# Kernel tuning notes

Hardware: AMD Instinct MI355X
Metric: run time of the kernel (lower is better)

## Reference

```python
import jax, jax.numpy as jnp
import numpy as np

N_NODES = 100000
N_EDGES = 1600000
IN_CH, HID, N_CLS = 768, 256, 8


def setup_inputs() -> dict:
    key = jax.random.key(0)
    k1, k2, k3, k4 = jax.random.split(key, 4)
    x = jax.random.normal(k1, (N_NODES, IN_CH), dtype=jnp.float32)
    edge_index = jax.random.randint(k2, (2, N_EDGES), 0, N_NODES, dtype=jnp.int64)
    # Glorot-ish init scaled for stability
    W1 = jax.random.normal(k3, (IN_CH, HID), dtype=jnp.float32) * (1.0 / np.sqrt(IN_CH))
    b1 = jnp.zeros((HID,), dtype=jnp.float32)
    W2 = jax.random.normal(k4, (HID, N_CLS), dtype=jnp.float32) * (1.0 / np.sqrt(HID))
    b2 = jnp.zeros((N_CLS,), dtype=jnp.float32)
    return {"x": x, "edge_index": edge_index, "W1": W1, "b1": b1, "W2": W2, "b2": b2}


def _gcn_norm(edge_index, num_nodes):
    # Add self-loops (PyG GCNConv default) and compute symmetric normalization.
    loops = jnp.arange(num_nodes, dtype=edge_index.dtype)
    row = jnp.concatenate([edge_index[0], loops])  # source nodes
    col = jnp.concatenate([edge_index[1], loops])  # target nodes
    ones = jnp.ones(col.shape[0], dtype=jnp.float32)
    deg = jax.ops.segment_sum(ones, col, num_segments=num_nodes)
    dinv = jnp.where(deg > 0, jax.lax.rsqrt(deg), 0.0)
    norm = dinv[row] * dinv[col]  # [E + N]
    return row, col, norm


def _gcn_conv(x, row, col, norm, W, b):
    h = x @ W                      # [N, out] dense transform first (out <= in)
    msg = h[row] * norm[:, None]    # gather + scale, [E+N, out]
    agg = jax.ops.segment_sum(msg, col, num_segments=x.shape[0])  # scatter-add
    return agg + b


def reference(x, edge_index, W1, b1, W2, b2):
    row, col, norm = _gcn_norm(edge_index, x.shape[0])
    h = _gcn_conv(x, row, col, norm, W1, b1)
    h = jax.nn.relu(h)
    # dropout is identity at eval (training=False)
    out = _gcn_conv(h, row, col, norm, W2, b2)
    return out
```

## Files before the change

### kernel.cpp

```cpp
#include <hip/hip_runtime.h>


#define NN 100000
#define NE 1600000
#define INC 768
#define HID 256
#define NCLS 8
#define NBLK 391

typedef short bf16x8 __attribute__((ext_vector_type(8)));
typedef float f32x4 __attribute__((ext_vector_type(4)));

__device__ __forceinline__ unsigned short f2bf(float f) {
  unsigned int u = __float_as_uint(f);
  unsigned int r = (u + 0x7FFFu + ((u >> 16) & 1u)) >> 16;
  return (unsigned short)r;
}
__device__ __forceinline__ float bf2f(unsigned short h) {
  return __uint_as_float(((unsigned int)h) << 16);
}

__global__ __launch_bounds__(256) void k_count(const int* __restrict__ ei, int* __restrict__ cnt) {
  int e = blockIdx.x * 256 + threadIdx.x;
  if (e < NE) atomicAdd(&cnt[ei[NE + e]], 1);
}

__global__ __launch_bounds__(256) void k_scan1(const int* __restrict__ cnt, int* __restrict__ bsum,
                                               float* __restrict__ dinv) {
  __shared__ int s[256];
  int i = blockIdx.x * 256 + threadIdx.x;
  int v = (i < NN) ? cnt[i] : 0;
  if (i < NN) dinv[i] = rsqrtf((float)v + 1.0f);
  s[threadIdx.x] = v;
  __syncthreads();
#pragma unroll
  for (int off = 128; off > 0; off >>= 1) {
    if (threadIdx.x < off) s[threadIdx.x] += s[threadIdx.x + off];
    __syncthreads();
  }
  if (threadIdx.x == 0) bsum[blockIdx.x] = s[0];
}
__global__ __launch_bounds__(512) void k_scan2(const int* __restrict__ bsum, int* __restrict__ boff,
                                               int* __restrict__ rowptr) {
  __shared__ int s[512];
  int tid = threadIdx.x;
  int v = (tid < NBLK) ? bsum[tid] : 0;
  s[tid] = v;
  __syncthreads();
#pragma unroll
  for (int off = 1; off < 512; off <<= 1) {
    int t = (tid >= off) ? s[tid - off] : 0;
    __syncthreads();
    s[tid] += t;
    __syncthreads();
  }
  if (tid < NBLK) boff[tid] = s[tid] - v;
  if (tid == NBLK - 1) rowptr[NN] = s[tid];
}
__global__ __launch_bounds__(256) void k_scan3(const int* __restrict__ cnt, const int* __restrict__ boff,
                                               int* __restrict__ rowptr, int* __restrict__ cursor) {
  __shared__ int s[256];
  int i = blockIdx.x * 256 + threadIdx.x;
  int v = (i < NN) ? cnt[i] : 0;
  s[threadIdx.x] = v;
  __syncthreads();
#pragma unroll
  for (int off = 1; off < 256; off <<= 1) {
    int t = (threadIdx.x >= off) ? s[threadIdx.x - off] : 0;
    __syncthreads();
    s[threadIdx.x] += t;
    __syncthreads();
  }
  if (i < NN) {
    int e = boff[blockIdx.x] + s[threadIdx.x] - v;
    rowptr[i] = e;
    cursor[i] = e;
  }
}
__global__ __launch_bounds__(256) void k_fill(const int* __restrict__ ei, const float* __restrict__ dinv,
                                              int* __restrict__ cursor, int2* __restrict__ epk) {
  int e = blockIdx.x * 256 + threadIdx.x;
  if (e >= NE) return;
  int r = ei[e];
  int c = ei[NE + e];
  float w = dinv[r] * dinv[c];
  int pos = atomicAdd(&cursor[c], 1);
  epk[pos] = make_int2(r, __float_as_int(w));
}

__global__ __launch_bounds__(256) void k_w1t(const float* __restrict__ W1, unsigned short* __restrict__ w1t) {
  int t = blockIdx.x * 256 + threadIdx.x;
  if (t >= INC * HID) return;
  int k = t / HID, n = t % HID;
  w1t[n * INC + k] = f2bf(W1[t]);
}

__global__ __launch_bounds__(512) void k_gemm1(const float* __restrict__ x,
                                               const unsigned short* __restrict__ w1t,
                                               unsigned short* __restrict__ h1) {
  __shared__ char smem[49152];
  unsigned short* As = (unsigned short*)smem;
  unsigned short* Bs = (unsigned short*)(smem + 16384);
  const int tid = threadIdx.x;
  const int lane = tid & 63;
  const int wid = tid >> 6;
  const int wm = wid >> 2;
  const int wn = wid & 3;
  const long bm = blockIdx.x;

  const int ar0 = tid >> 3, as7 = tid & 7;
  const int ar1 = (tid + 512) >> 3;
  long arow0 = bm * 128 + ar0; if (arow0 > NN - 1) arow0 = NN - 1;
  long arow1 = bm * 128 + ar1; if (arow1 > NN - 1) arow1 = NN - 1;
  const float* gA0 = x + arow0 * INC + as7 * 8;
  const float* gA1 = x + arow1 * INC + as7 * 8;
  const int aoff0 = (ar0 << 7) | ((as7 ^ (ar0 & 7)) << 4);
  const int aoff1 = (ar1 << 7) | ((as7 ^ (ar1 & 7)) << 4);

  f32x4 acc[4][4];
#pragma unroll
  for (int m = 0; m < 4; m++)
#pragma unroll
    for (int n = 0; n < 4; n++) acc[m][n] = (f32x4){0.f, 0.f, 0.f, 0.f};

  float4 fa00, fa01, fa10, fa11;
  uint4 rb0, rb1, rb2, rb3;

#define LOAD_AB(KT)                                                        \
  do {                                                                     \
    fa00 = *(const float4*)(gA0 + (KT));                                   \
    fa01 = *(const float4*)(gA0 + (KT) + 4);                               \
    fa10 = *(const float4*)(gA1 + (KT));                                   \
    fa11 = *(const float4*)(gA1 + (KT) + 4);                               \
    rb0 = *(const uint4*)(w1t + (long)(tid >> 3) * INC + (KT) + (tid & 7) * 8);            \
    rb1 = *(const uint4*)(w1t + (long)((tid + 512) >> 3) * INC + (KT) + (tid & 7) * 8);    \
    rb2 = *(const uint4*)(w1t + (long)((tid + 1024) >> 3) * INC + (KT) + (tid & 7) * 8);   \
    rb3 = *(const uint4*)(w1t + (long)((tid + 1536) >> 3) * INC + (KT) + (tid & 7) * 8);   \
  } while (0)

  LOAD_AB(0);

  for (int kt = 0; kt < INC; kt += 64) {
    {
      union { unsigned short us[8]; uint4 v; } u;
      u.us[0] = f2bf(fa00.x); u.us[1] = f2bf(fa00.y); u.us[2] = f2bf(fa00.z); u.us[3] = f2bf(fa00.w);
      u.us[4] = f2bf(fa01.x); u.us[5] = f2bf(fa01.y); u.us[6] = f2bf(fa01.z); u.us[7] = f2bf(fa01.w);
      *(uint4*)((char*)As + aoff0) = u.v;
      u.us[0] = f2bf(fa10.x); u.us[1] = f2bf(fa10.y); u.us[2] = f2bf(fa10.z); u.us[3] = f2bf(fa10.w);
      u.us[4] = f2bf(fa11.x); u.us[5] = f2bf(fa11.y); u.us[6] = f2bf(fa11.z); u.us[7] = f2bf(fa11.w);
      *(uint4*)((char*)As + aoff1) = u.v;
    }
    {
      int r0 = tid >> 3, s7 = tid & 7;
      *(uint4*)((char*)Bs + ((r0 << 7) | ((s7 ^ (r0 & 7)) << 4))) = rb0;
      int r1 = (tid + 512) >> 3;
      *(uint4*)((char*)Bs + ((r1 << 7) | ((s7 ^ (r1 & 7)) << 4))) = rb1;
      int r2 = (tid + 1024) >> 3;
      *(uint4*)((char*)Bs + ((r2 << 7) | ((s7 ^ (r2 & 7)) << 4))) = rb2;
      int r3 = (tid + 1536) >> 3;
      *(uint4*)((char*)Bs + ((r3 << 7) | ((s7 ^ (r3 & 7)) << 4))) = rb3;
    }
    __syncthreads();
    if (kt + 64 < INC) LOAD_AB(kt + 64);
#pragma unroll
    for (int half = 0; half < 2; half++) {
      bf16x8 af[4], bff[4];
      int j = (half << 2) + (lane >> 4);
#pragma unroll
      for (int m = 0; m < 4; m++) {
        int row = wm * 64 + m * 16 + (lane & 15);
        int off = (row << 7) | ((j ^ (row & 7)) << 4);
        af[m] = *(const bf16x8*)((const char*)As + off);
      }
#pragma unroll
      for (int n = 0; n < 4; n++) {
        int row = wn * 64 + n * 16 + (lane & 15);
        int off = (row << 7) | ((j ^ (row & 7)) << 4);
        bff[n] = *(const bf16x8*)((const char*)Bs + off);
      }
#pragma unroll
      for (int m = 0; m < 4; m++)
#pragma unroll
        for (int n = 0; n < 4; n++)
          acc[m][n] = __builtin_amdgcn_mfma_f32_16x16x32_bf16(af[m], bff[n], acc[m][n], 0, 0, 0);
    }
    __syncthreads();
  }
#undef LOAD_AB

  unsigned short* Os = (unsigned short*)smem;
#pragma unroll
  for (int chunk = 0; chunk < 2; chunk++) {
    if (wm == chunk) {
#pragma unroll
      for (int m = 0; m < 4; m++)
#pragma unroll
        for (int n = 0; n < 4; n++) {
          int lrow = m * 16 + ((lane >> 4) << 2);
          int lcol = wn * 64 + n * 16 + (lane & 15);
#pragma unroll
          for (int r = 0; r < 4; r++)
            Os[(lrow + r) * 264 + lcol] = f2bf(acc[m][n][r]);
        }
    }
    __syncthreads();
    {
      int r = tid >> 3, s = tid & 7;
      long grow = bm * 128 + chunk * 64 + r;
      if (grow < NN) {
        unsigned short* dst = h1 + grow * HID;
#pragma unroll
        for (int i = 0; i < 4; i++) {
          int seg = s + i * 8;
          *(uint4*)(dst + seg * 8) = *(const uint4*)((const char*)Os + (long)r * 528 + seg * 16);
        }
      }
    }
    __syncthreads();
  }
}

__global__ __launch_bounds__(256) void k_agg1(const unsigned short* __restrict__ h1,
                                              const float* __restrict__ dinv,
                                              const int* __restrict__ rowptr,
                                              const int2* __restrict__ epk,
                                              const float* __restrict__ b1,
                                              const float* __restrict__ W2,
                                              float* __restrict__ h2) {
  int w = (int)((blockIdx.x * 256 + threadIdx.x) >> 6);
  int lane = threadIdx.x & 63;
  if (w >= NN) return;
  float di = dinv[w];
  int c4 = lane << 2;
  const unsigned short* hb = h1 + c4;
  ushort4 hv = *(const ushort4*)(hb + (long)w * HID);
  float self = di * di;
  float a0 = self * bf2f(hv.x), a1 = self * bf2f(hv.y);
  float a2 = self * bf2f(hv.z), a3 = self * bf2f(hv.w);
  int e = rowptr[w], e1 = rowptr[w + 1];
  if ((e & 1) && e < e1) {
    int2 q = epk[e];
    float ws = __int_as_float(q.y);
    ushort4 g = *(const ushort4*)(hb + (long)q.x * HID);
    a0 += ws * bf2f(g.x); a1 += ws * bf2f(g.y);
    a2 += ws * bf2f(g.z); a3 += ws * bf2f(g.w);
    e++;
  }
  for (; e + 8 <= e1; e += 8) {
    uint4 p0 = *(const uint4*)(epk + e);
    uint4 p1 = *(const uint4*)(epk + e + 2);
    uint4 p2 = *(const uint4*)(epk + e + 4);
    uint4 p3 = *(const uint4*)(epk + e + 6);
    ushort4 g0 = *(const ushort4*)(hb + (long)(int)p0.x * HID);
    ushort4 g1 = *(const ushort4*)(hb + (long)(int)p0.z * HID);
    ushort4 g2 = *(const ushort4*)(hb + (long)(int)p1.x * HID);
    ushort4 g3 = *(const ushort4*)(hb + (long)(int)p1.z * HID);
    ushort4 g4 = *(const ushort4*)(hb + (long)(int)p2.x * HID);
    ushort4 g5 = *(const ushort4*)(hb + (long)(int)p2.z * HID);
    ushort4 g6 = *(const ushort4*)(hb + (long)(int)p3.x * HID);
    ushort4 g7 = *(const ushort4*)(hb + (long)(int)p3.z * HID);
    float w0 = __uint_as_float(p0.y), w1 = __uint_as_float(p0.w);
    float w2 = __uint_as_float(p1.y), w3 = __uint_as_float(p1.w);
    float w4 = __uint_as_float(p2.y), w5 = __uint_as_float(p2.w);
    float w6 = __uint_as_float(p3.y), w7 = __uint_as_float(p3.w);
    a0 += w0 * bf2f(g0.x) + w1 * bf2f(g1.x) + w2 * bf2f(g2.x) + w3 * bf2f(g3.x) +
          w4 * bf2f(g4.x) + w5 * bf2f(g5.x) + w6 * bf2f(g6.x) + w7 * bf2f(g7.x);
    a1 += w0 * bf2f(g0.y) + w1 * bf2f(g1.y) + w2 * bf2f(g2.y) + w3 * bf2f(g3.y) +
          w4 * bf2f(g4.y) + w5 * bf2f(g5.y) + w6 * bf2f(g6.y) + w7 * bf2f(g7.y);
    a2 += w0 * bf2f(g0.z) + w1 * bf2f(g1.z) + w2 * bf2f(g2.z) + w3 * bf2f(g3.z) +
          w4 * bf2f(g4.z) + w5 * bf2f(g5.z) + w6 * bf2f(g6.z) + w7 * bf2f(g7.z);
    a3 += w0 * bf2f(g0.w) + w1 * bf2f(g1.w) + w2 * bf2f(g2.w) + w3 * bf2f(g3.w) +
          w4 * bf2f(g4.w) + w5 * bf2f(g5.w) + w6 * bf2f(g6.w) + w7 * bf2f(g7.w);
  }
  for (; e + 2 <= e1; e += 2) {
    uint4 p = *(const uint4*)(epk + e);
    ushort4 g0 = *(const ushort4*)(hb + (long)(int)p.x * HID);
    ushort4 g1 = *(const ushort4*)(hb + (long)(int)p.z * HID);
    float w0 = __uint_as_float(p.y), w1 = __uint_as_float(p.w);
    a0 += w0 * bf2f(g0.x) + w1 * bf2f(g1.x);
    a1 += w0 * bf2f(g0.y) + w1 * bf2f(g1.y);
    a2 += w0 * bf2f(g0.z) + w1 * bf2f(g1.z);
    a3 += w0 * bf2f(g0.w) + w1 * bf2f(g1.w);
  }
  if (e < e1) {
    int2 q = epk[e];
    float ws = __int_as_float(q.y);
    ushort4 g = *(const ushort4*)(hb + (long)q.x * HID);
    a0 += ws * bf2f(g.x); a1 += ws * bf2f(g.y);
    a2 += ws * bf2f(g.z); a3 += ws * bf2f(g.w);
  }
  float4 bv = *(const float4*)(b1 + c4);
  float v0 = a0 + bv.x; v0 = v0 > 0.f ? v0 : 0.f;
  float v1 = a1 + bv.y; v1 = v1 > 0.f ? v1 : 0.f;
  float v2 = a2 + bv.z; v2 = v2 > 0.f ? v2 : 0.f;
  float v3 = a3 + bv.w; v3 = v3 > 0.f ? v3 : 0.f;
  const float4* wp = (const float4*)(W2 + ((long)c4 << 3));
  float4 r0a = wp[0], r0b = wp[1], r1a = wp[2], r1b = wp[3];
  float4 r2a = wp[4], r2b = wp[5], r3a = wp[6], r3b = wp[7];
  float p[8];
  p[0] = v0 * r0a.x + v1 * r1a.x + v2 * r2a.x + v3 * r3a.x;
  p[1] = v0 * r0a.y + v1 * r1a.y + v2 * r2a.y + v3 * r3a.y;
  p[2] = v0 * r0a.z + v1 * r1a.z + v2 * r2a.z + v3 * r3a.z;
  p[3] = v0 * r0a.w + v1 * r1a.w + v2 * r2a.w + v3 * r3a.w;
  p[4] = v0 * r0b.x + v1 * r1b.x + v2 * r2b.x + v3 * r3b.x;
  p[5] = v0 * r0b.y + v1 * r1b.y + v2 * r2b.y + v3 * r3b.y;
  p[6] = v0 * r0b.z + v1 * r1b.z + v2 * r2b.z + v3 * r3b.z;
  p[7] = v0 * r0b.w + v1 * r1b.w + v2 * r2b.w + v3 * r3b.w;
#pragma unroll
  for (int c = 0; c < 8; c++)
#pragma unroll
    for (int off = 1; off < 64; off <<= 1) p[c] += __shfl_xor(p[c], off, 64);
  if (lane < 8) {
    float o = p[0];
    o = (lane == 1) ? p[1] : o;
    o = (lane == 2) ? p[2] : o;
    o = (lane == 3) ? p[3] : o;
    o = (lane == 4) ? p[4] : o;
    o = (lane == 5) ? p[5] : o;
    o = (lane == 6) ? p[6] : o;
    o = (lane == 7) ? p[7] : o;
    h2[(long)w * NCLS + lane] = o;
  }
}

__global__ __launch_bounds__(256) void k_agg2(const float* __restrict__ h2,
                                              const float* __restrict__ dinv,
                                              const int* __restrict__ rowptr,
                                              const int2* __restrict__ epk,
                                              const float* __restrict__ b2,
                                              float* __restrict__ out) {
  long t = (long)blockIdx.x * 256 + threadIdx.x;
  long i = t >> 3;
  int c = (int)(t & 7);
  if (i >= NN) return;
  float di = dinv[i];
  float s = di * di * h2[i * NCLS + c];
  int e = rowptr[i], e1 = rowptr[i + 1];
  for (; e + 8 <= e1; e += 8) {
    int2 q0 = epk[e],     q1 = epk[e + 1], q2 = epk[e + 2], q3 = epk[e + 3];
    int2 q4 = epk[e + 4], q5 = epk[e + 5], q6 = epk[e + 6], q7 = epk[e + 7];
    float g0 = h2[(long)q0.x * NCLS + c], g1 = h2[(long)q1.x * NCLS + c];
    float g2 = h2[(long)q2.x * NCLS + c], g3 = h2[(long)q3.x * NCLS + c];
    float g4 = h2[(long)q4.x * NCLS + c], g5 = h2[(long)q5.x * NCLS + c];
    float g6 = h2[(long)q6.x * NCLS + c], g7 = h2[(long)q7.x * NCLS + c];
    s += __int_as_float(q0.y) * g0 + __int_as_float(q1.y) * g1 +
         __int_as_float(q2.y) * g2 + __int_as_float(q3.y) * g3 +
         __int_as_float(q4.y) * g4 + __int_as_float(q5.y) * g5 +
         __int_as_float(q6.y) * g6 + __int_as_float(q7.y) * g7;
  }
  for (; e < e1; e++) {
    int2 q = epk[e];
    s += __int_as_float(q.y) * h2[(long)q.x * NCLS + c];
  }
  out[i * NCLS + c] = s + b2[c];
}

extern "C" void kernel_launch(void* const* d_in, const int* in_sizes, int n_in,
                              void* d_out, int out_size, void* d_ws, size_t ws_size,
                              hipStream_t stream) {
  (void)in_sizes; (void)n_in; (void)out_size; (void)ws_size;
  const float* x  = (const float*)d_in[0];
  const int*   ei = (const int*)d_in[1];
  const float* W1 = (const float*)d_in[2];
  const float* b1 = (const float*)d_in[3];
  const float* W2 = (const float*)d_in[4];
  const float* b2 = (const float*)d_in[5];
  float* out = (float*)d_out;
  char* ws = (char*)d_ws;

  unsigned short* h1   = (unsigned short*)(ws + 0L);
  float* h2            = (float*)(ws + 51200000L);
  float* dinv          = (float*)(ws + 54400000L);
  int*   cnt           = (int*)(ws + 54800000L);
  int*   rowptr        = (int*)(ws + 55200000L);
  int*   cursor        = (int*)(ws + 55600128L);
  int2*  epk           = (int2*)(ws + 56000128L);
  unsigned short* w1t  = (unsigned short*)(ws + 68800128L);
  int*   bsum          = (int*)(ws + 69195008L);
  int*   boff          = (int*)(ws + 69196608L);

  hipMemsetAsync(cnt, 0, NN * sizeof(int), stream);
  k_count<<<(NE + 255) / 256, 256, 0, stream>>>(ei, cnt);
  k_scan1<<<NBLK, 256, 0, stream>>>(cnt, bsum, dinv);
  k_scan2<<<1, 512, 0, stream>>>(bsum, boff, rowptr);
  k_scan3<<<NBLK, 256, 0, stream>>>(cnt, boff, rowptr, cursor);
  k_fill<<<(NE + 255) / 256, 256, 0, stream>>>(ei, dinv, cursor, epk);
  k_w1t<<<(INC * HID + 255) / 256, 256, 0, stream>>>(W1, w1t);
  k_gemm1<<<782, 512, 0, stream>>>(x, w1t, h1);
  k_agg1<<<(NN * 64 + 255) / 256, 256, 0, stream>>>(h1, dinv, rowptr, epk, b1, W2, h2);
  k_agg2<<<(NN * NCLS + 255) / 256, 256, 0, stream>>>(h2, dinv, rowptr, epk, b2, out);
}
```

Before: 458.0 us.

## Double-buffer GEMM1 LDS tiles with half-size K steps

Splits the 64-wide K tile of the first GEMM into two 32-wide tiles held in separate LDS buffers. Each one is written while MFMAs run on the other, so staging overlaps compute and the barrier wait between store and compute shrinks. Register prefetch now holds half as much data per thread, which lowers register pressure. In exchange the LDS swizzle is narrower, and the kernel issues more barriers and smaller global loads per iteration.

```diff
diff --git a/kernel.cpp b/kernel.cpp
--- a/kernel.cpp
+++ b/kernel.cpp
@@ -99,8 +99,10 @@
                                                const unsigned short* __restrict__ w1t,
                                                unsigned short* __restrict__ h1) {
   __shared__ char smem[49152];
-  unsigned short* As = (unsigned short*)smem;
-  unsigned short* Bs = (unsigned short*)(smem + 16384);
+  unsigned short* A0 = (unsigned short*)smem;
+  unsigned short* A1 = (unsigned short*)(smem + 8192);
+  unsigned short* B0 = (unsigned short*)(smem + 16384);
+  unsigned short* B1 = (unsigned short*)(smem + 32768);
   const int tid = threadIdx.x;
   const int lane = tid & 63;
   const int wid = tid >> 6;
@@ -108,14 +110,16 @@
   const int wn = wid & 3;
   const long bm = blockIdx.x;
 
-  const int ar0 = tid >> 3, as7 = tid & 7;
-  const int ar1 = (tid + 512) >> 3;
-  long arow0 = bm * 128 + ar0; if (arow0 > NN - 1) arow0 = NN - 1;
-  long arow1 = bm * 128 + ar1; if (arow1 > NN - 1) arow1 = NN - 1;
-  const float* gA0 = x + arow0 * INC + as7 * 8;
-  const float* gA1 = x + arow1 * INC + as7 * 8;
-  const int aoff0 = (ar0 << 7) | ((as7 ^ (ar0 & 7)) << 4);
-  const int aoff1 = (ar1 << 7) | ((as7 ^ (ar1 & 7)) << 4);
+  const int ar = tid >> 2, ak = tid & 3;
+  long arow = bm * 128 + ar; if (arow > NN - 1) arow = NN - 1;
+  const float* gA = x + arow * INC + ak * 8;
+  const int aoff = (ar << 6) | ((ak ^ (ar & 3)) << 4);
+  const int br0 = tid >> 2;
+  const int br1 = (tid + 512) >> 2;
+  const unsigned short* gB0 = w1t + (long)br0 * INC + ak * 8;
+  const unsigned short* gB1 = w1t + (long)br1 * INC + ak * 8;
+  const int boff0 = (br0 << 6) | ((ak ^ (br0 & 3)) << 4);
+  const int boff1 = (br1 << 6) | ((ak ^ (br1 & 3)) << 4);
 
   f32x4 acc[4][4];
 #pragma unroll
@@ -123,70 +127,70 @@
 #pragma unroll
     for (int n = 0; n < 4; n++) acc[m][n] = (f32x4){0.f, 0.f, 0.f, 0.f};
 
-  float4 fa00, fa01, fa10, fa11;
-  uint4 rb0, rb1, rb2, rb3;
-
-#define LOAD_AB(KT)                                                        \
-  do {                                                                     \
-    fa00 = *(const float4*)(gA0 + (KT));                                   \
-    fa01 = *(const float4*)(gA0 + (KT) + 4);                               \
-    fa10 = *(const float4*)(gA1 + (KT));                                   \
-    fa11 = *(const float4*)(gA1 + (KT) + 4);                               \
-    rb0 = *(const uint4*)(w1t + (long)(tid >> 3) * INC + (KT) + (tid & 7) * 8);            \
-    rb1 = *(const uint4*)(w1t + (long)((tid + 512) >> 3) * INC + (KT) + (tid & 7) * 8);    \
-    rb2 = *(const uint4*)(w1t + (long)((tid + 1024) >> 3) * INC + (KT) + (tid & 7) * 8);   \
-    rb3 = *(const uint4*)(w1t + (long)((tid + 1536) >> 3) * INC + (KT) + (tid & 7) * 8);   \
+  float4 fa0, fa1;
+  uint4 rb0, rb1;
+
+#define LOAD_T(KT)                              \
+  do {                                          \
+    fa0 = *(const float4*)(gA + (KT));          \
+    fa1 = *(const float4*)(gA + (KT) + 4);      \
+    rb0 = *(const uint4*)(gB0 + (KT));          \
+    rb1 = *(const uint4*)(gB1 + (KT));          \
   } while (0)
 
-  LOAD_AB(0);
-
-  for (int kt = 0; kt < INC; kt += 64) {
-    {
-      union { unsigned short us[8]; uint4 v; } u;
-      u.us[0] = f2bf(fa00.x); u.us[1] = f2bf(fa00.y); u.us[2] = f2bf(fa00.z); u.us[3] = f2bf(fa00.w);
-      u.us[4] = f2bf(fa01.x); u.us[5] = f2bf(fa01.y); u.us[6] = f2bf(fa01.z); u.us[7] = f2bf(fa01.w);
-      *(uint4*)((char*)As + aoff0) = u.v;
-      u.us[0] = f2bf(fa10.x); u.us[1] = f2bf(fa10.y); u.us[2] = f2bf(fa10.z); u.us[3] = f2bf(fa10.w);
-      u.us[4] = f2bf(fa11.x); u.us[5] = f2bf(fa11.y); u.us[6] = f2bf(fa11.z); u.us[7] = f2bf(fa11.w);
-      *(uint4*)((char*)As + aoff1) = u.v;
+#define WRITE_T(AB, BB)                                                          \
+  do {                                                                           \
+    union { unsigned short us[8]; uint4 v; } u;                                  \
+    u.us[0] = f2bf(fa0.x); u.us[1] = f2bf(fa0.y); u.us[2] = f2bf(fa0.z);         \
+    u.us[3] = f2bf(fa0.w); u.us[4] = f2bf(fa1.x); u.us[5] = f2bf(fa1.y);         \
+    u.us[6] = f2bf(fa1.z); u.us[7] = f2bf(fa1.w);                                \
+    *(uint4*)((char*)(AB) + aoff) = u.v;                                         \
+    *(uint4*)((char*)(BB) + boff0) = rb0;                                        \
+    *(uint4*)((char*)(BB) + boff1) = rb1;                                        \
+  } while (0)
+
+#define MFMA_T(AB, BB)                                                           \
+  do {                                                                           \
+    bf16x8 af[4], bff[4];                                                        \
+    int j = lane >> 4;                                                           \
+    _Pragma("unroll")                                                            \
+    for (int m = 0; m < 4; m++) {                                                \
+      int row = wm * 64 + m * 16 + (lane & 15);                                  \
+      af[m] = *(const bf16x8*)((const char*)(AB) + ((row << 6) | ((j ^ (row & 3)) << 4))); \
+    }                                                                            \
+    _Pragma("unroll")                                                            \
+    for (int n = 0; n < 4; n++) {                                                \
+      int row = wn * 64 + n * 16 + (lane & 15);                                  \
+      bff[n] = *(const bf16x8*)((const char*)(BB) + ((row << 6) | ((j ^ (row & 3)) << 4))); \
+    }                                                                            \
+    _Pragma("unroll")                                                            \
+    for (int m = 0; m < 4; m++)                                                  \
+      _Pragma("unroll")                                                          \
+      for (int n = 0; n < 4; n++)                                                \
+        acc[m][n] = __builtin_amdgcn_mfma_f32_16x16x32_bf16(af[m], bff[n], acc[m][n], 0, 0, 0); \
+  } while (0)
+
+  LOAD_T(0);
+  WRITE_T(A0, B0);
+  LOAD_T(32);
+  __syncthreads();
+
+  for (int u = 0; u < 12; u++) {
+    int kt = u * 64;
+    WRITE_T(A1, B1);
+    if (kt + 64 < INC) LOAD_T(kt + 64);
+    MFMA_T(A0, B0);
+    __syncthreads();
+    if (kt + 64 < INC) {
+      WRITE_T(A0, B0);
+      if (kt + 96 < INC) LOAD_T(kt + 96);
     }
-    {
-      int r0 = tid >> 3, s7 = tid & 7;
-      *(uint4*)((char*)Bs + ((r0 << 7) | ((s7 ^ (r0 & 7)) << 4))) = rb0;
-      int r1 = (tid + 512) >> 3;
-      *(uint4*)((char*)Bs + ((r1 << 7) | ((s7 ^ (r1 & 7)) << 4))) = rb1;
-      int r2 = (tid + 1024) >> 3;
-      *(uint4*)((char*)Bs + ((r2 << 7) | ((s7 ^ (r2 & 7)) << 4))) = rb2;
-      int r3 = (tid + 1536) >> 3;
-      *(uint4*)((char*)Bs + ((r3 << 7) | ((s7 ^ (r3 & 7)) << 4))) = rb3;
-    }
-    __syncthreads();
-    if (kt + 64 < INC) LOAD_AB(kt + 64);
-#pragma unroll
-    for (int half = 0; half < 2; half++) {
-      bf16x8 af[4], bff[4];
-      int j = (half << 2) + (lane >> 4);
-#pragma unroll
-      for (int m = 0; m < 4; m++) {
-        int row = wm * 64 + m * 16 + (lane & 15);
-        int off = (row << 7) | ((j ^ (row & 7)) << 4);
-        af[m] = *(const bf16x8*)((const char*)As + off);
-      }
-#pragma unroll
-      for (int n = 0; n < 4; n++) {
-        int row = wn * 64 + n * 16 + (lane & 15);
-        int off = (row << 7) | ((j ^ (row & 7)) << 4);
-        bff[n] = *(const bf16x8*)((const char*)Bs + off);
-      }
-#pragma unroll
-      for (int m = 0; m < 4; m++)
-#pragma unroll
-        for (int n = 0; n < 4; n++)
-          acc[m][n] = __builtin_amdgcn_mfma_f32_16x16x32_bf16(af[m], bff[n], acc[m][n], 0, 0, 0);
-    }
-    __syncthreads();
-  }
-#undef LOAD_AB
+    MFMA_T(A1, B1);
+    __syncthreads();
+  }
+#undef LOAD_T
+#undef WRITE_T
+#undef MFMA_T
 
   unsigned short* Os = (unsigned short*)smem;
 #pragma unroll
```

Measured after the change: 482.3 us. 1.05x slower.

## Restructure GEMM1 to stream W1 from global in MFMA-ready layout, no LDS staging

Applied to the files above, without the earlier changes.

The first GEMM no longer stages A and B tiles through shared memory with barriers. Each wave now owns 16 rows and all 256 output columns. It reads x directly into registers and loads W1 fragments from global memory, using a new pre-packed [k/8][n][8] layout that matches the MFMA operand shape. This removes the LDS traffic and the __syncthreads per k-tile. In exchange, every wave re-reads the whole of W1 from L2/cache, uses 64 accumulator registers, and gets less B reuse per block. The bf16 conversion now uses the HIP intrinsic instead of hand-written rounding.

```diff
diff --git a/kernel.cpp b/kernel.cpp
--- a/kernel.cpp
+++ b/kernel.cpp
@@ -1,4 +1,5 @@
 #include <hip/hip_runtime.h>
+#include <hip/hip_bf16.h>
 
 
 #define NN 100000
@@ -12,9 +13,8 @@
 typedef float f32x4 __attribute__((ext_vector_type(4)));
 
 __device__ __forceinline__ unsigned short f2bf(float f) {
-  unsigned int u = __float_as_uint(f);
-  unsigned int r = (u + 0x7FFFu + ((u >> 16) & 1u)) >> 16;
-  return (unsigned short)r;
+  __hip_bfloat16 h = __float2bfloat16(f);
+  return *reinterpret_cast<unsigned short*>(&h);
 }
 __device__ __forceinline__ float bf2f(unsigned short h) {
   return __uint_as_float(((unsigned int)h) << 16);
@@ -88,135 +88,70 @@
   epk[pos] = make_int2(r, __float_as_int(w));
 }
 
-__global__ __launch_bounds__(256) void k_w1t(const float* __restrict__ W1, unsigned short* __restrict__ w1t) {
+__global__ __launch_bounds__(256) void k_w1t(const float* __restrict__ W1, unsigned short* __restrict__ w1t2) {
   int t = blockIdx.x * 256 + threadIdx.x;
   if (t >= INC * HID) return;
   int k = t / HID, n = t % HID;
-  w1t[n * INC + k] = f2bf(W1[t]);
-}
-
-__global__ __launch_bounds__(512) void k_gemm1(const float* __restrict__ x,
-                                               const unsigned short* __restrict__ w1t,
+  w1t2[(k >> 3) * (HID * 8) + n * 8 + (k & 7)] = f2bf(W1[t]);
+}
+
+__global__ __launch_bounds__(256) void k_gemm1(const float* __restrict__ x,
+                                               const unsigned short* __restrict__ w1t2,
                                                unsigned short* __restrict__ h1) {
-  __shared__ char smem[49152];
-  unsigned short* As = (unsigned short*)smem;
-  unsigned short* Bs = (unsigned short*)(smem + 16384);
+  __shared__ unsigned short Os[64 * 264];
   const int tid = threadIdx.x;
   const int lane = tid & 63;
-  const int wid = tid >> 6;
-  const int wm = wid >> 2;
-  const int wn = wid & 3;
-  const long bm = blockIdx.x;
-
-  const int ar0 = tid >> 3, as7 = tid & 7;
-  const int ar1 = (tid + 512) >> 3;
-  long arow0 = bm * 128 + ar0; if (arow0 > NN - 1) arow0 = NN - 1;
-  long arow1 = bm * 128 + ar1; if (arow1 > NN - 1) arow1 = NN - 1;
-  const float* gA0 = x + arow0 * INC + as7 * 8;
-  const float* gA1 = x + arow1 * INC + as7 * 8;
-  const int aoff0 = (ar0 << 7) | ((as7 ^ (ar0 & 7)) << 4);
-  const int aoff1 = (ar1 << 7) | ((as7 ^ (ar1 & 7)) << 4);
-
-  f32x4 acc[4][4];
-#pragma unroll
-  for (int m = 0; m < 4; m++)
-#pragma unroll
-    for (int n = 0; n < 4; n++) acc[m][n] = (f32x4){0.f, 0.f, 0.f, 0.f};
-
-  float4 fa00, fa01, fa10, fa11;
-  uint4 rb0, rb1, rb2, rb3;
-
-#define LOAD_AB(KT)                                                        \
-  do {                                                                     \
-    fa00 = *(const float4*)(gA0 + (KT));                                   \
-    fa01 = *(const float4*)(gA0 + (KT) + 4);                               \
-    fa10 = *(const float4*)(gA1 + (KT));                                   \
-    fa11 = *(const float4*)(gA1 + (KT) + 4);                               \
-    rb0 = *(const uint4*)(w1t + (long)(tid >> 3) * INC + (KT) + (tid & 7) * 8);            \
-    rb1 = *(const uint4*)(w1t + (long)((tid + 512) >> 3) * INC + (KT) + (tid & 7) * 8);    \
-    rb2 = *(const uint4*)(w1t + (long)((tid + 1024) >> 3) * INC + (KT) + (tid & 7) * 8);   \
-    rb3 = *(const uint4*)(w1t + (long)((tid + 1536) >> 3) * INC + (KT) + (tid & 7) * 8);   \
-  } while (0)
-
-  LOAD_AB(0);
-
-  for (int kt = 0; kt < INC; kt += 64) {
-    {
-      union { unsigned short us[8]; uint4 v; } u;
-      u.us[0] = f2bf(fa00.x); u.us[1] = f2bf(fa00.y); u.us[2] = f2bf(fa00.z); u.us[3] = f2bf(fa00.w);
-      u.us[4] = f2bf(fa01.x); u.us[5] = f2bf(fa01.y); u.us[6] = f2bf(fa01.z); u.us[7] = f2bf(fa01.w);
-      *(uint4*)((char*)As + aoff0) = u.v;
-      u.us[0] = f2bf(fa10.x); u.us[1] = f2bf(fa10.y); u.us[2] = f2bf(fa10.z); u.us[3] = f2bf(fa10.w);
-      u.us[4] = f2bf(fa11.x); u.us[5] = f2bf(fa11.y); u.us[6] = f2bf(fa11.z); u.us[7] = f2bf(fa11.w);
-      *(uint4*)((char*)As + aoff1) = u.v;
+  const int wv = tid >> 6;
+  const int j = lane >> 4;
+  const int rr = lane & 15;
+  long row = (long)blockIdx.x * 64 + wv * 16 + rr;
+  if (row > NN - 1) row = NN - 1;
+  const float* ga = x + row * INC + j * 8;
+
+  f32x4 acc[16];
+#pragma unroll
+  for (int n = 0; n < 16; n++) acc[n] = (f32x4){0.f, 0.f, 0.f, 0.f};
+
+  float4 a0 = *(const float4*)(ga);
+  float4 a1 = *(const float4*)(ga + 4);
+
+  const unsigned short* gb2 = w1t2 + (long)j * (HID * 8) + rr * 8;
+
+#pragma unroll
+  for (int kk = 0; kk < INC; kk += 32) {
+    union { unsigned short us[8]; bf16x8 v; } ua;
+    ua.us[0] = f2bf(a0.x); ua.us[1] = f2bf(a0.y); ua.us[2] = f2bf(a0.z); ua.us[3] = f2bf(a0.w);
+    ua.us[4] = f2bf(a1.x); ua.us[5] = f2bf(a1.y); ua.us[6] = f2bf(a1.z); ua.us[7] = f2bf(a1.w);
+    bf16x8 af = ua.v;
+    if (kk + 32 < INC) {
+      a0 = *(const float4*)(ga + kk + 32);
+      a1 = *(const float4*)(ga + kk + 36);
     }
-    {
-      int r0 = tid >> 3, s7 = tid & 7;
-      *(uint4*)((char*)Bs + ((r0 << 7) | ((s7 ^ (r0 & 7)) << 4))) = rb0;
-      int r1 = (tid + 512) >> 3;
-      *(uint4*)((char*)Bs + ((r1 << 7) | ((s7 ^ (r1 & 7)) << 4))) = rb1;
-      int r2 = (tid + 1024) >> 3;
-      *(uint4*)((char*)Bs + ((r2 << 7) | ((s7 ^ (r2 & 7)) << 4))) = rb2;
-      int r3 = (tid + 1536) >> 3;
-      *(uint4*)((char*)Bs + ((r3 << 7) | ((s7 ^ (r3 & 7)) << 4))) = rb3;
+#pragma unroll
+    for (int n = 0; n < 16; n++) {
+      bf16x8 bv = *(const bf16x8*)(gb2 + n * 128);
+      acc[n] = __builtin_amdgcn_mfma_f32_16x16x32_bf16(af, bv, acc[n], 0, 0, 0);
     }
-    __syncthreads();
-    if (kt + 64 < INC) LOAD_AB(kt + 64);
-#pragma unroll
-    for (int half = 0; half < 2; half++) {
-      bf16x8 af[4], bff[4];
-      int j = (half << 2) + (lane >> 4);
-#pragma unroll
-      for (int m = 0; m < 4; m++) {
-        int row = wm * 64 + m * 16 + (lane & 15);
-        int off = (row << 7) | ((j ^ (row & 7)) << 4);
-        af[m] = *(const bf16x8*)((const char*)As + off);
-      }
-#pragma unroll
-      for (int n = 0; n < 4; n++) {
-        int row = wn * 64 + n * 16 + (lane & 15);
-        int off = (row << 7) | ((j ^ (row & 7)) << 4);
-        bff[n] = *(const bf16x8*)((const char*)Bs + off);
-      }
-#pragma unroll
-      for (int m = 0; m < 4; m++)
-#pragma unroll
-        for (int n = 0; n < 4; n++)
-          acc[m][n] = __builtin_amdgcn_mfma_f32_16x16x32_bf16(af[m], bff[n], acc[m][n], 0, 0, 0);
-    }
-    __syncthreads();
-  }
-#undef LOAD_AB
-
-  unsigned short* Os = (unsigned short*)smem;
-#pragma unroll
-  for (int chunk = 0; chunk < 2; chunk++) {
-    if (wm == chunk) {
-#pragma unroll
-      for (int m = 0; m < 4; m++)
-#pragma unroll
-        for (int n = 0; n < 4; n++) {
-          int lrow = m * 16 + ((lane >> 4) << 2);
-          int lcol = wn * 64 + n * 16 + (lane & 15);
-#pragma unroll
-          for (int r = 0; r < 4; r++)
-            Os[(lrow + r) * 264 + lcol] = f2bf(acc[m][n][r]);
-        }
-    }
-    __syncthreads();
-    {
-      int r = tid >> 3, s = tid & 7;
-      long grow = bm * 128 + chunk * 64 + r;
-      if (grow < NN) {
-        unsigned short* dst = h1 + grow * HID;
-#pragma unroll
-        for (int i = 0; i < 4; i++) {
-          int seg = s + i * 8;
-          *(uint4*)(dst + seg * 8) = *(const uint4*)((const char*)Os + (long)r * 528 + seg * 16);
-        }
-      }
-    }
-    __syncthreads();
+    gb2 += 4 * (HID * 8);
+  }
+
+#pragma unroll
+  for (int n = 0; n < 16; n++) {
+    int lrow = wv * 16 + j * 4;
+    int lcol = n * 16 + rr;
+#pragma unroll
+    for (int r = 0; r < 4; r++)
+      Os[(lrow + r) * 264 + lcol] = f2bf(acc[n][r]);
+  }
+  __syncthreads();
+#pragma unroll
+  for (int i = 0; i < 8; i++) {
+    int idx = i * 256 + tid;
+    int r = idx >> 5;
+    int q = idx & 31;
+    long grow = (long)blockIdx.x * 64 + r;
+    if (grow < NN)
+      *(uint4*)(h1 + grow * HID + q * 8) = *(const uint4*)((const char*)Os + (long)r * 528 + q * 16);
   }
 }
 
@@ -375,7 +310,7 @@
   int*   rowptr        = (int*)(ws + 55200000L);
   int*   cursor        = (int*)(ws + 55600128L);
   int2*  epk           = (int2*)(ws + 56000128L);
-  unsigned short* w1t  = (unsigned short*)(ws + 68800128L);
+  unsigned short* w1t2 = (unsigned short*)(ws + 68800128L);
   int*   bsum          = (int*)(ws + 69195008L);
   int*   boff          = (int*)(ws + 69196608L);
 
@@ -385,8 +320,8 @@
   k_scan2<<<1, 512, 0, stream>>>(bsum, boff, rowptr);
   k_scan3<<<NBLK, 256, 0, stream>>>(cnt, boff, rowptr, cursor);
   k_fill<<<(NE + 255) / 256, 256, 0, stream>>>(ei, dinv, cursor, epk);
-  k_w1t<<<(INC * HID + 255) / 256, 256, 0, stream>>>(W1, w1t);
-  k_gemm1<<<782, 512, 0, stream>>>(x, w1t, h1);
+  k_w1t<<<(INC * HID + 255) / 256, 256, 0, stream>>>(W1, w1t2);
+  k_gemm1<<<(NN + 63) / 64, 256, 0, stream>>>(x, w1t2, h1);
   k_agg1<<<(NN * 64 + 255) / 256, 256, 0, stream>>>(h1, dinv, rowptr, epk, b1, W2, h2);
   k_agg2<<<(NN * NCLS + 255) / 256, 256, 0, stream>>>(h2, dinv, rowptr, epk, b2, out);
 }
```

Measured after the change: 622.5 us. +35.9%, slower.
